# Performance work log

Measured on AMD Instinct MI355X. Metric: run time of the kernel, lower is better.

Reference implementation:

```python
import jax, jax.numpy as jnp
import numpy as np

BZ, T, D, DFF, E, BEAMS = 128, 32, 768, 3072, 8, 2


def setup_inputs() -> dict:
    key = jax.random.key(0)
    ks = jax.random.split(key, 4)
    s = 0.02
    return {
        "x": jax.random.normal(ks[0], (BZ, T, D), jnp.float32),
        "attention_mask": jnp.ones((BZ, T), jnp.float32),
        "Wg": jax.random.normal(ks[1], (D, E), jnp.float32) * s,   # gate Linear(D,E,bias=False)
        "W1": jax.random.normal(ks[2], (E, D, DFF), jnp.float32) * s,
        "b1": jnp.zeros((E, DFF), jnp.float32),
        "W2": jax.random.normal(ks[3], (E, DFF, D), jnp.float32) * s,
        "b2": jnp.zeros((E, D), jnp.float32),
    }


def reference(x, attention_mask, Wg, W1, b1, W2, b2):
    # forward_gate: module builds its own all-ones mask regardless of input mask
    mask = jnp.ones((x.shape[0], x.shape[1]), x.dtype)
    x_avg = (x * mask[..., None]).sum(1) / mask[..., None].sum(1)   # [bz, D]
    prob = jax.nn.softmax(x_avg @ Wg, axis=-1)                       # [bz, E]
    # beam_search (layer_judge='first', pre-route): topk on exp(log(softmax)) == softmax probs
    scores = jnp.exp(jnp.log(prob))
    topv, topi = jax.lax.top_k(scores, BEAMS)                        # [bz, beams]
    beam_scores = topv.reshape(-1)                                   # [bz*beams]
    expert_route = topi.reshape(-1, 1)                                # [bz*beams, 1]
    sel = expert_route[:, -1]
    # replicate x per beam: [bz*beams, T, D]
    x_rep = jnp.broadcast_to(x[:, None], (x.shape[0], BEAMS, x.shape[1], x.shape[2]))
    x_rep = x_rep.reshape(-1, x.shape[1], x.shape[2])
    # per-sample expert FFN dispatch (dense masked loop over the E=8 experts)
    out = jnp.zeros_like(x_rep)
    for e in range(E):
        h = jax.nn.gelu(jnp.einsum('nsd,df->nsf', x_rep, W1[e]) + b1[e], approximate=False)
        ye = jnp.einsum('nsf,fd->nsd', h, W2[e]) + b2[e]
        out = jnp.where((sel == e)[:, None, None], ye, out)
    return (out, beam_scores, expert_route)
```

## Files before the change

### kernel.cpp

```cpp
#include <hip/hip_runtime.h>
#include <cstddef>
#include <cstdint>

#define BZd   128
#define Td    32
#define Dd    768
#define DFFd  3072
#define Ed    8
#define NBEAM 256
#define ROWS_TOT 8192
#define OUT_ELEMS 6291456
#define MAXTILES 72
#define MAXT2    40

typedef unsigned short u16;
typedef __attribute__((ext_vector_type(4))) unsigned short ushort4v;
typedef __attribute__((ext_vector_type(8))) short frag_ab;
typedef __attribute__((ext_vector_type(4))) float floatx4;

__device__ __forceinline__ u16 f2bf(float f) {
  unsigned int u = __builtin_bit_cast(unsigned int, f);
  u += 0x7FFFu + ((u >> 16) & 1u);
  return (u16)(u >> 16);
}

__device__ __forceinline__ void async_copy16(u16* lds, const u16* g) {
  __builtin_amdgcn_global_load_lds(
      (const __attribute__((address_space(1))) void*)g,
      (__attribute__((address_space(3))) void*)lds, 16, 0, 0);
}

__device__ __forceinline__ float gelu_fast(float x) {
  float z = 1.5957691216f * (x + 0.044715f * x * x * x);
  return x / (1.0f + __expf(-z));
}

__global__ __launch_bounds__(256) void route_kernel(
    const float* __restrict__ x, const float* __restrict__ Wg,
    float* __restrict__ out, int* __restrict__ sel) {
  int b = blockIdx.x;
  int t = threadIdx.x;
  __shared__ float red[256][8];
  float la[8];
#pragma unroll
  for (int e = 0; e < 8; e++) la[e] = 0.f;
  for (int d = t; d < Dd; d += 256) {
    const float* xp = x + (size_t)b * Td * Dd + d;
    float xa = 0.f;
#pragma unroll
    for (int tt = 0; tt < Td; tt++) xa += xp[(size_t)tt * Dd];
    xa *= (1.0f / 32.0f);
#pragma unroll
    for (int e = 0; e < 8; e++) la[e] += xa * Wg[d * 8 + e];
  }
#pragma unroll
  for (int e = 0; e < 8; e++) red[t][e] = la[e];
  __syncthreads();
  for (int s = 128; s > 0; s >>= 1) {
    if (t < s) {
#pragma unroll
      for (int e = 0; e < 8; e++) red[t][e] += red[t + s][e];
    }
    __syncthreads();
  }
  if (t == 0) {
    float lg[8];
#pragma unroll
    for (int e = 0; e < 8; e++) lg[e] = red[0][e];
    float mx = lg[0];
#pragma unroll
    for (int e = 1; e < 8; e++) mx = fmaxf(mx, lg[e]);
    float p[8];
    float sum = 0.f;
#pragma unroll
    for (int e = 0; e < 8; e++) { p[e] = __expf(lg[e] - mx); sum += p[e]; }
    float inv = 1.0f / sum;
#pragma unroll
    for (int e = 0; e < 8; e++) p[e] *= inv;
    int i0 = 0; float v0 = p[0];
#pragma unroll
    for (int e = 1; e < 8; e++) if (p[e] > v0) { v0 = p[e]; i0 = e; }
    int i1 = -1; float v1 = -1.0f;
#pragma unroll
    for (int e = 0; e < 8; e++) if (e != i0 && p[e] > v1) { v1 = p[e]; i1 = e; }
    float* bs = out + OUT_ELEMS;
    float* er = out + OUT_ELEMS + NBEAM;
    bs[2 * b] = v0; bs[2 * b + 1] = v1;
    er[2 * b] = (float)i0; er[2 * b + 1] = (float)i1;
    sel[2 * b] = i0; sel[2 * b + 1] = i1;
  }
}

__global__ __launch_bounds__(256) void bucket_kernel(
    const int* __restrict__ sel, int* __restrict__ perm,
    int4* __restrict__ tiles, int4* __restrict__ tiles2) {
  __shared__ int ssel[NBEAM];
  __shared__ int scnt[8];
  __shared__ int soff[8];
  __shared__ int scur[8];
  __shared__ int sperm[NBEAM];
  int t = threadIdx.x;
  ssel[t] = sel[t];
  __syncthreads();
  if (t == 0) {
    for (int e = 0; e < 8; e++) scnt[e] = 0;
    for (int n = 0; n < NBEAM; n++) scnt[ssel[n]]++;
    int o = 0;
    for (int e = 0; e < 8; e++) { soff[e] = o; scur[e] = o; o += scnt[e]; }
    for (int n = 0; n < NBEAM; n++) { int e = ssel[n]; sperm[scur[e]++] = n; }
    int tt = 0;
    for (int e = 0; e < 8; e++) {
      int nr = scnt[e] * 32;
      int base = soff[e] * 32;
      for (int r0 = 0; r0 < nr; r0 += 128) {
        tiles[tt] = make_int4(e, base + r0, min(128, nr - r0), 0);
        tt++;
      }
    }
    for (; tt < MAXTILES; tt++) tiles[tt] = make_int4(-1, 0, 0, 0);
    int t2 = 0;
    for (int e = 0; e < 8; e++) {
      int nr = scnt[e] * 32;
      int base = soff[e] * 32;
      for (int r0 = 0; r0 < nr; r0 += 256) {
        tiles2[t2] = make_int4(e, base + r0, min(256, nr - r0), 0);
        t2++;
      }
    }
    for (; t2 < MAXT2; t2++) tiles2[t2] = make_int4(-1, 0, 0, 0);
  }
  __syncthreads();
  perm[t] = sperm[t];
}

__global__ __launch_bounds__(256) void convert_x_kernel(
    const float* __restrict__ x, u16* __restrict__ xbf) {
  size_t i = ((size_t)blockIdx.x * 256 + threadIdx.x) * 4;
  float4 v = *(const float4*)(x + i);
  ushort4v pv = {f2bf(v.x), f2bf(v.y), f2bf(v.z), f2bf(v.w)};
  *(ushort4v*)(xbf + i) = pv;
}

__global__ __launch_bounds__(256) void transpose_bf16_kernel(
    const float* __restrict__ in, u16* __restrict__ out, int row0, int col0,
    int ld_in, size_t estr_in, int ld_out, size_t estr_out) {
  __shared__ u16 tile[64][65];
  int e = blockIdx.z;
  int r0 = blockIdx.x * 64, c0 = blockIdx.y * 64;
  int t = threadIdx.x;
  int rr = t >> 4, cc4 = (t & 15) * 4;
  const float* ip = in + (size_t)e * estr_in + (size_t)(row0 + r0) * ld_in + col0 + c0;
#pragma unroll
  for (int i = 0; i < 4; i++) {
    int r = rr + 16 * i;
    float4 v = *(const float4*)(ip + (size_t)r * ld_in + cc4);
    tile[r][cc4 + 0] = f2bf(v.x);
    tile[r][cc4 + 1] = f2bf(v.y);
    tile[r][cc4 + 2] = f2bf(v.z);
    tile[r][cc4 + 3] = f2bf(v.w);
  }
  __syncthreads();
  int ccw = t >> 4, r4 = (t & 15) * 4;
  u16* op = out + (size_t)e * estr_out + (size_t)c0 * ld_out + r0;
#pragma unroll
  for (int i = 0; i < 4; i++) {
    int cc = ccw + 16 * i;
    ushort4v pv = {tile[r4 + 0][cc], tile[r4 + 1][cc], tile[r4 + 2][cc], tile[r4 + 3][cc]};
    *(ushort4v*)(op + (size_t)cc * ld_out + r4) = pv;
  }
}

__global__ __launch_bounds__(512, 2) void gemm1_kernel(
    const u16* __restrict__ xbf, const u16* __restrict__ w1t,
    const float* __restrict__ b1, const int* __restrict__ perm,
    const int4* __restrict__ tiles2, u16* __restrict__ h, int f0, int FC) {
  int4 meta = tiles2[blockIdx.y];
  int e = meta.x;
  if (e < 0) return;
  int grow0 = meta.y, nrows = meta.z;
  int bx = blockIdx.x;

  extern __shared__ __align__(16) u16 smem[];
  u16* As = smem;
  u16* Bs = smem + 32768;

  int t = threadIdx.x;
  int l = t & 63;
  int wid = t >> 6;
  int wr = wid >> 2;
  int wc = wid & 3;
  int lrow = l & 15, lquad = l >> 4;

  const u16* ag[4]; const u16* bg[4];
  int ldst[4];
#pragma unroll
  for (int j = 0; j < 4; j++) {
    int s = j * 512 + t;
    int m = s >> 3;
    int koff = ((s & 7) ^ ((m >> 1) & 7)) * 8;
    int gr = grow0 + m;
    int bidx = gr >> 5; bidx = bidx < NBEAM ? bidx : NBEAM - 1;
    int batch = perm[bidx] >> 1;
    ag[j] = xbf + ((size_t)batch * Td + (m & 31)) * Dd + koff;
    bg[j] = w1t + ((size_t)e * FC + bx * 256 + m) * Dd + koff;
    ldst[j] = j * 4096 + t * 8;
  }

  int swz = (lrow >> 1) & 7;
  int ca0 = (lquad ^ swz) * 8, ca1 = ((lquad + 4) ^ swz) * 8;
  int abase0 = (wr * 128 + lrow) * 64 + ca0;
  int abase1 = (wr * 128 + lrow) * 64 + ca1;
  int bbase0 = (wc * 64 + lrow) * 64 + ca0;
  int bbase1 = (wc * 64 + lrow) * 64 + ca1;

  floatx4 acc[8][4];
#pragma unroll
  for (int mi = 0; mi < 8; mi++)
#pragma unroll
    for (int ni = 0; ni < 4; ni++) acc[mi][ni] = (floatx4){0.f, 0.f, 0.f, 0.f};

  const int nk = Dd / 64;

#pragma unroll
  for (int j = 0; j < 4; j++) { async_copy16(As + ldst[j], ag[j]); ag[j] += 64; }
#pragma unroll
  for (int j = 0; j < 4; j++) { async_copy16(Bs + ldst[j], bg[j]); bg[j] += 64; }

  for (int kt = 0; kt < nk; kt++) {
    const int b = kt & 1;
    const u16* Ab = As + b * 16384;
    const u16* Bb = Bs + b * 16384;
    const int pd = (b ^ 1) * 16384;
    const bool pre = (kt + 1 < nk);

    frag_ab af[4], bfr[4];

    if (pre) {
      async_copy16(As + pd + ldst[0], ag[0]); ag[0] += 64;
      async_copy16(As + pd + ldst[1], ag[1]); ag[1] += 64;
      asm volatile("s_waitcnt vmcnt(2)\n\ts_barrier" ::: "memory");
    } else {
      asm volatile("s_waitcnt vmcnt(0)\n\ts_barrier" ::: "memory");
    }
#pragma unroll
    for (int i = 0; i < 4; i++) bfr[i] = *(const frag_ab*)(Bb + bbase0 + i * 1024);
#pragma unroll
    for (int i = 0; i < 4; i++) af[i] = *(const frag_ab*)(Ab + abase0 + i * 1024);
    __builtin_amdgcn_s_setprio(1);
#pragma unroll
    for (int mi = 0; mi < 4; mi++)
#pragma unroll
      for (int ni = 0; ni < 4; ni++)
        acc[mi][ni] = __builtin_amdgcn_mfma_f32_16x16x32_bf16(bfr[ni], af[mi], acc[mi][ni], 0, 0, 0);
    __builtin_amdgcn_s_setprio(0);

    if (pre) {
      async_copy16(As + pd + ldst[2], ag[2]); ag[2] += 64;
      async_copy16(As + pd + ldst[3], ag[3]); ag[3] += 64;
    }
#pragma unroll
    for (int i = 0; i < 4; i++) af[i] = *(const frag_ab*)(Ab + abase0 + (i + 4) * 1024);
    __builtin_amdgcn_s_setprio(1);
#pragma unroll
    for (int mi = 0; mi < 4; mi++)
#pragma unroll
      for (int ni = 0; ni < 4; ni++)
        acc[mi + 4][ni] = __builtin_amdgcn_mfma_f32_16x16x32_bf16(bfr[ni], af[mi], acc[mi + 4][ni], 0, 0, 0);
    __builtin_amdgcn_s_setprio(0);

    if (pre) {
      async_copy16(Bs + pd + ldst[0], bg[0]); bg[0] += 64;
      async_copy16(Bs + pd + ldst[1], bg[1]); bg[1] += 64;
    }
#pragma unroll
    for (int i = 0; i < 4; i++) bfr[i] = *(const frag_ab*)(Bb + bbase1 + i * 1024);
#pragma unroll
    for (int i = 0; i < 4; i++) af[i] = *(const frag_ab*)(Ab + abase1 + i * 1024);
    __builtin_amdgcn_s_setprio(1);
#pragma unroll
    for (int mi = 0; mi < 4; mi++)
#pragma unroll
      for (int ni = 0; ni < 4; ni++)
        acc[mi][ni] = __builtin_amdgcn_mfma_f32_16x16x32_bf16(bfr[ni], af[mi], acc[mi][ni], 0, 0, 0);
    __builtin_amdgcn_s_setprio(0);

    if (pre) {
      async_copy16(Bs + pd + ldst[2], bg[2]); bg[2] += 64;
      async_copy16(Bs + pd + ldst[3], bg[3]); bg[3] += 64;
    }
#pragma unroll
    for (int i = 0; i < 4; i++) af[i] = *(const frag_ab*)(Ab + abase1 + (i + 4) * 1024);
    __builtin_amdgcn_s_setprio(1);
#pragma unroll
    for (int mi = 0; mi < 4; mi++)
#pragma unroll
      for (int ni = 0; ni < 4; ni++)
        acc[mi + 4][ni] = __builtin_amdgcn_mfma_f32_16x16x32_bf16(bfr[ni], af[mi], acc[mi + 4][ni], 0, 0, 0);
    __builtin_amdgcn_s_setprio(0);

    asm volatile("s_barrier" ::: "memory");
  }

#pragma unroll
  for (int mi = 0; mi < 8; mi++) {
    int row = wr * 128 + mi * 16 + lrow;
    if (row < nrows) {
      u16* hp = h + (size_t)(grow0 + row) * FC + bx * 256 + wc * 64 + lquad * 4;
      const float* bp = b1 + (size_t)e * DFFd + f0 + bx * 256 + wc * 64 + lquad * 4;
#pragma unroll
      for (int ni = 0; ni < 4; ni++) {
        float4 bias = *(const float4*)(bp + ni * 16);
        ushort4v pv = {f2bf(gelu_fast(acc[mi][ni][0] + bias.x)),
                       f2bf(gelu_fast(acc[mi][ni][1] + bias.y)),
                       f2bf(gelu_fast(acc[mi][ni][2] + bias.z)),
                       f2bf(gelu_fast(acc[mi][ni][3] + bias.w))};
        *(ushort4v*)(hp + ni * 16) = pv;
      }
    }
  }
}

__global__ __launch_bounds__(512, 2) void gemm2_kernel(
    const u16* __restrict__ h, const u16* __restrict__ w2t,
    const float* __restrict__ b2, const int* __restrict__ perm,
    const int4* __restrict__ tiles2, float* __restrict__ out,
    float* __restrict__ part, int FC, int first) {
  int4 meta = tiles2[blockIdx.y];
  int e = meta.x;
  if (e < 0) return;
  int grow0 = meta.y, nrows = meta.z;
  int bx = blockIdx.x;
  int kz = blockIdx.z;
  const int KC = FC / (int)gridDim.z;

  extern __shared__ __align__(16) u16 smem[];
  u16* As = smem;
  u16* Bs = smem + 32768;
  __shared__ int sbeam[8];

  int t = threadIdx.x;
  if (t < 8) {
    int idx = (grow0 >> 5) + t;
    sbeam[t] = perm[idx < NBEAM ? idx : NBEAM - 1];
  }
  __syncthreads();

  int l = t & 63;
  int wid = t >> 6;
  int wr = wid >> 2;
  int wc = wid & 3;
  int lrow = l & 15, lquad = l >> 4;

  const u16* ag[4]; const u16* bg[4];
  int ldst[4];
#pragma unroll
  for (int j = 0; j < 4; j++) {
    int s = j * 512 + t;
    int m = s >> 3;
    int koff = ((s & 7) ^ ((m >> 1) & 7)) * 8;
    int arow = grow0 + m;
    arow = arow < ROWS_TOT ? arow : ROWS_TOT - 1;
    ag[j] = h + (size_t)arow * FC + kz * KC + koff;
    bg[j] = w2t + ((size_t)e * Dd + bx * 256 + m) * FC + kz * KC + koff;
    ldst[j] = j * 4096 + t * 8;
  }

  int swz = (lrow >> 1) & 7;
  int ca0 = (lquad ^ swz) * 8, ca1 = ((lquad + 4) ^ swz) * 8;
  int abase0 = (wr * 128 + lrow) * 64 + ca0;
  int abase1 = (wr * 128 + lrow) * 64 + ca1;
  int bbase0 = (wc * 64 + lrow) * 64 + ca0;
  int bbase1 = (wc * 64 + lrow) * 64 + ca1;

  floatx4 acc[8][4];
#pragma unroll
  for (int mi = 0; mi < 8; mi++)
#pragma unroll
    for (int ni = 0; ni < 4; ni++) acc[mi][ni] = (floatx4){0.f, 0.f, 0.f, 0.f};

  const int nk = KC / 64;

#pragma unroll
  for (int j = 0; j < 4; j++) { async_copy16(As + ldst[j], ag[j]); ag[j] += 64; }
#pragma unroll
  for (int j = 0; j < 4; j++) { async_copy16(Bs + ldst[j], bg[j]); bg[j] += 64; }

  for (int kt = 0; kt < nk; kt++) {
    const int b = kt & 1;
    const u16* Ab = As + b * 16384;
    const u16* Bb = Bs + b * 16384;
    const int pd = (b ^ 1) * 16384;
    const bool pre = (kt + 1 < nk);

    frag_ab af[4], bfr[4];

    if (pre) {
      async_copy16(As + pd + ldst[0], ag[0]); ag[0] += 64;
      async_copy16(As + pd + ldst[1], ag[1]); ag[1] += 64;
      asm volatile("s_waitcnt vmcnt(2)\n\ts_barrier" ::: "memory");
    } else {
      asm volatile("s_waitcnt vmcnt(0)\n\ts_barrier" ::: "memory");
    }
#pragma unroll
    for (int i = 0; i < 4; i++) bfr[i] = *(const frag_ab*)(Bb + bbase0 + i * 1024);
#pragma unroll
    for (int i = 0; i < 4; i++) af[i] = *(const frag_ab*)(Ab + abase0 + i * 1024);
    __builtin_amdgcn_s_setprio(1);
#pragma unroll
    for (int mi = 0; mi < 4; mi++)
#pragma unroll
      for (int ni = 0; ni < 4; ni++)
        acc[mi][ni] = __builtin_amdgcn_mfma_f32_16x16x32_bf16(bfr[ni], af[mi], acc[mi][ni], 0, 0, 0);
    __builtin_amdgcn_s_setprio(0);

    if (pre) {
      async_copy16(As + pd + ldst[2], ag[2]); ag[2] += 64;
      async_copy16(As + pd + ldst[3], ag[3]); ag[3] += 64;
    }
#pragma unroll
    for (int i = 0; i < 4; i++) af[i] = *(const frag_ab*)(Ab + abase0 + (i + 4) * 1024);
    __builtin_amdgcn_s_setprio(1);
#pragma unroll
    for (int mi = 0; mi < 4; mi++)
#pragma unroll
      for (int ni = 0; ni < 4; ni++)
        acc[mi + 4][ni] = __builtin_amdgcn_mfma_f32_16x16x32_bf16(bfr[ni], af[mi], acc[mi + 4][ni], 0, 0, 0);
    __builtin_amdgcn_s_setprio(0);

    if (pre) {
      async_copy16(Bs + pd + ldst[0], bg[0]); bg[0] += 64;
      async_copy16(Bs + pd + ldst[1], bg[1]); bg[1] += 64;
    }
#pragma unroll
    for (int i = 0; i < 4; i++) bfr[i] = *(const frag_ab*)(Bb + bbase1 + i * 1024);
#pragma unroll
    for (int i = 0; i < 4; i++) af[i] = *(const frag_ab*)(Ab + abase1 + i * 1024);
    __builtin_amdgcn_s_setprio(1);
#pragma unroll
    for (int mi = 0; mi < 4; mi++)
#pragma unroll
      for (int ni = 0; ni < 4; ni++)
        acc[mi][ni] = __builtin_amdgcn_mfma_f32_16x16x32_bf16(bfr[ni], af[mi], acc[mi][ni], 0, 0, 0);
    __builtin_amdgcn_s_setprio(0);

    if (pre) {
      async_copy16(Bs + pd + ldst[2], bg[2]); bg[2] += 64;
      async_copy16(Bs + pd + ldst[3], bg[3]); bg[3] += 64;
    }
#pragma unroll
    for (int i = 0; i < 4; i++) af[i] = *(const frag_ab*)(Ab + abase1 + (i + 4) * 1024);
    __builtin_amdgcn_s_setprio(1);
#pragma unroll
    for (int mi = 0; mi < 4; mi++)
#pragma unroll
      for (int ni = 0; ni < 4; ni++)
        acc[mi + 4][ni] = __builtin_amdgcn_mfma_f32_16x16x32_bf16(bfr[ni], af[mi], acc[mi + 4][ni], 0, 0, 0);
    __builtin_amdgcn_s_setprio(0);

    asm volatile("s_barrier" ::: "memory");
  }

#pragma unroll
  for (int mi = 0; mi < 8; mi++) {
    int row = wr * 128 + mi * 16 + lrow;
    if (row < nrows) {
      int beam = sbeam[row >> 5];
      size_t base = ((size_t)beam * Td + (row & 31)) * Dd + bx * 256 + wc * 64 + lquad * 4;
      float* op = (kz == 0 ? out : part) + base;
      const float* bp = b2 + (size_t)e * Dd + bx * 256 + wc * 64 + lquad * 4;
#pragma unroll
      for (int ni = 0; ni < 4; ni++) {
        if (first) {
          float4 v = {acc[mi][ni][0], acc[mi][ni][1], acc[mi][ni][2], acc[mi][ni][3]};
          if (kz == 0) {
            float4 bias = *(const float4*)(bp + ni * 16);
            v.x += bias.x; v.y += bias.y; v.z += bias.z; v.w += bias.w;
          }
          *(float4*)(op + ni * 16) = v;
        } else {
          float4 o = *(float4*)(op + ni * 16);
          o.x += acc[mi][ni][0]; o.y += acc[mi][ni][1];
          o.z += acc[mi][ni][2]; o.w += acc[mi][ni][3];
          *(float4*)(op + ni * 16) = o;
        }
      }
    }
  }
}

__global__ __launch_bounds__(256) void reduce_kernel(
    float* __restrict__ out, const float* __restrict__ part) {
  size_t i = ((size_t)blockIdx.x * 256 + threadIdx.x) * 4;
  float4 o = *(float4*)(out + i);
  float4 p = *(const float4*)(part + i);
  o.x += p.x; o.y += p.y; o.z += p.z; o.w += p.w;
  *(float4*)(out + i) = o;
}

extern "C" void kernel_launch(void* const* d_in, const int* in_sizes, int n_in,
                              void* d_out, int out_size, void* d_ws, size_t ws_size,
                              hipStream_t stream) {
  const float* x  = (const float*)d_in[0];
  const float* Wg = (const float*)d_in[2];
  const float* W1 = (const float*)d_in[3];
  const float* b1 = (const float*)d_in[4];
  const float* W2 = (const float*)d_in[5];
  const float* b2 = (const float*)d_in[6];
  float* out = (float*)d_out;

  char* ws = (char*)d_ws;
  int*  sel    = (int*)ws;
  int*  perm   = sel + NBEAM;
  int4* tiles  = (int4*)(ws + 4096);
  int4* tiles2 = (int4*)(ws + 6144);

  const size_t xbf_off = 65536;
  const size_t xbf_bytes = (size_t)BZd * Td * Dd * 2;
  int FC = 768;
  if      (xbf_off + xbf_bytes + (size_t)40960 * 3072 <= ws_size) FC = 3072;
  else if (xbf_off + xbf_bytes + (size_t)40960 * 1536 <= ws_size) FC = 1536;
  int NC = DFFd / FC;

  u16* xbf = (u16*)(ws + xbf_off);
  u16* w1t = (u16*)(ws + xbf_off + xbf_bytes);
  u16* w2t = w1t + (size_t)Ed * FC * Dd;
  u16* h   = w2t + (size_t)Ed * Dd * FC;

  const size_t part_off = xbf_off + xbf_bytes + (size_t)40960 * FC;
  const size_t part_bytes = (size_t)OUT_ELEMS * 4;
  int SPLIT = (part_off + part_bytes <= ws_size) ? 2 : 1;
  float* part = (float*)(ws + part_off);

  static bool attr_done = false;
  if (!attr_done) {
    hipFuncSetAttribute(reinterpret_cast<const void*>(gemm1_kernel),
                        hipFuncAttributeMaxDynamicSharedMemorySize, 131072);
    hipFuncSetAttribute(reinterpret_cast<const void*>(gemm2_kernel),
                        hipFuncAttributeMaxDynamicSharedMemorySize, 131072);
    attr_done = true;
  }

  route_kernel<<<BZd, 256, 0, stream>>>(x, Wg, out, sel);
  bucket_kernel<<<1, 256, 0, stream>>>(sel, perm, tiles, tiles2);
  convert_x_kernel<<<(BZd * Td * Dd) / 1024, 256, 0, stream>>>(x, xbf);

  for (int c = 0; c < NC; c++) {
    transpose_bf16_kernel<<<dim3(Dd / 64, FC / 64, Ed), 256, 0, stream>>>(
        W1, w1t, 0, c * FC, DFFd, (size_t)Dd * DFFd, Dd, (size_t)FC * Dd);
    transpose_bf16_kernel<<<dim3(FC / 64, Dd / 64, Ed), 256, 0, stream>>>(
        W2, w2t, c * FC, 0, Dd, (size_t)DFFd * Dd, FC, (size_t)Dd * FC);
    gemm1_kernel<<<dim3(FC / 256, MAXT2), 512, 131072, stream>>>(
        xbf, w1t, b1, perm, tiles2, h, c * FC, FC);
    gemm2_kernel<<<dim3(Dd / 256, MAXT2, SPLIT), 512, 131072, stream>>>(
        h, w2t, b2, perm, tiles2, out, part, FC, c == 0 ? 1 : 0);
  }
  if (SPLIT == 2)
    reduce_kernel<<<OUT_ELEMS / 1024, 256, 0, stream>>>(out, part);
}
```

Baseline: 371.7 us.

## Use 1024-thread GEMM blocks, merge weight transposes, fuse x conversion into routing

The two expert GEMM kernels now run 16 waves per block instead of 8. Each wave owns a 64x64 output sub-tile rather than 128x64, which halves the accumulator registers per thread and doubles the number of waves available to hide latency for the same 256x256 tile. The W1 and W2 transposes are merged into one launch, and the fp32-to-bf16 conversion of x moves into the routing kernel, removing two kernel launches. The risks are higher LDS barrier contention and a longer tail in the routing kernel, which now also streams the full activation tensor.

Result: faster. 364.1 us (-2.1%).

```diff
diff --git a/kernel.cpp b/kernel.cpp
--- a/kernel.cpp
+++ b/kernel.cpp
@@ -37,7 +37,7 @@
 
 __global__ __launch_bounds__(256) void route_kernel(
     const float* __restrict__ x, const float* __restrict__ Wg,
-    float* __restrict__ out, int* __restrict__ sel) {
+    float* __restrict__ out, int* __restrict__ sel, u16* __restrict__ xbf) {
   int b = blockIdx.x;
   int t = threadIdx.x;
   __shared__ float red[256][8];
@@ -89,11 +89,18 @@
     er[2 * b] = (float)i0; er[2 * b + 1] = (float)i1;
     sel[2 * b] = i0; sel[2 * b + 1] = i1;
   }
+  const float* xs = x + (size_t)b * Td * Dd;
+  u16* xd = xbf + (size_t)b * Td * Dd;
+  for (int i = t; i < Td * Dd / 4; i += 256) {
+    float4 v = *(const float4*)(xs + (size_t)i * 4);
+    ushort4v pv = {f2bf(v.x), f2bf(v.y), f2bf(v.z), f2bf(v.w)};
+    *(ushort4v*)(xd + (size_t)i * 4) = pv;
+  }
 }
 
 __global__ __launch_bounds__(256) void bucket_kernel(
     const int* __restrict__ sel, int* __restrict__ perm,
-    int4* __restrict__ tiles, int4* __restrict__ tiles2) {
+    int4* __restrict__ tiles2) {
   __shared__ int ssel[NBEAM];
   __shared__ int scnt[8];
   __shared__ int soff[8];
@@ -108,16 +115,6 @@
     int o = 0;
     for (int e = 0; e < 8; e++) { soff[e] = o; scur[e] = o; o += scnt[e]; }
     for (int n = 0; n < NBEAM; n++) { int e = ssel[n]; sperm[scur[e]++] = n; }
-    int tt = 0;
-    for (int e = 0; e < 8; e++) {
-      int nr = scnt[e] * 32;
-      int base = soff[e] * 32;
-      for (int r0 = 0; r0 < nr; r0 += 128) {
-        tiles[tt] = make_int4(e, base + r0, min(128, nr - r0), 0);
-        tt++;
-      }
-    }
-    for (; tt < MAXTILES; tt++) tiles[tt] = make_int4(-1, 0, 0, 0);
     int t2 = 0;
     for (int e = 0; e < 8; e++) {
       int nr = scnt[e] * 32;
@@ -133,20 +130,27 @@
   perm[t] = sperm[t];
 }
 
-__global__ __launch_bounds__(256) void convert_x_kernel(
-    const float* __restrict__ x, u16* __restrict__ xbf) {
-  size_t i = ((size_t)blockIdx.x * 256 + threadIdx.x) * 4;
-  float4 v = *(const float4*)(x + i);
-  ushort4v pv = {f2bf(v.x), f2bf(v.y), f2bf(v.z), f2bf(v.w)};
-  *(ushort4v*)(xbf + i) = pv;
-}
-
-__global__ __launch_bounds__(256) void transpose_bf16_kernel(
-    const float* __restrict__ in, u16* __restrict__ out, int row0, int col0,
-    int ld_in, size_t estr_in, int ld_out, size_t estr_out) {
+__global__ __launch_bounds__(256) void transpose2_kernel(
+    const float* __restrict__ W1, const float* __restrict__ W2,
+    u16* __restrict__ w1t, u16* __restrict__ w2t, int c, int FC) {
   __shared__ u16 tile[64][65];
-  int e = blockIdx.z;
-  int r0 = blockIdx.x * 64, c0 = blockIdx.y * 64;
+  int z = blockIdx.z;
+  const float* in; u16* out;
+  int e, r0, c0, row0, col0, ld_in, ld_out;
+  size_t estr_in, estr_out;
+  if (z < 8) {
+    e = z; in = W1; out = w1t;
+    row0 = 0; col0 = c * FC; ld_in = DFFd; estr_in = (size_t)Dd * DFFd;
+    ld_out = Dd; estr_out = (size_t)FC * Dd;
+    r0 = blockIdx.y * 64;
+    c0 = blockIdx.x * 64;
+  } else {
+    e = z - 8; in = W2; out = w2t;
+    row0 = c * FC; col0 = 0; ld_in = Dd; estr_in = (size_t)DFFd * Dd;
+    ld_out = FC; estr_out = (size_t)Dd * FC;
+    r0 = blockIdx.x * 64;
+    c0 = blockIdx.y * 64;
+  }
   int t = threadIdx.x;
   int rr = t >> 4, cc4 = (t & 15) * 4;
   const float* ip = in + (size_t)e * estr_in + (size_t)(row0 + r0) * ld_in + col0 + c0;
@@ -170,7 +174,7 @@
   }
 }
 
-__global__ __launch_bounds__(512, 2) void gemm1_kernel(
+__global__ __launch_bounds__(1024, 4) void gemm1_kernel(
     const u16* __restrict__ xbf, const u16* __restrict__ w1t,
     const float* __restrict__ b1, const int* __restrict__ perm,
     const int4* __restrict__ tiles2, u16* __restrict__ h, int f0, int FC) {
@@ -191,40 +195,39 @@
   int wc = wid & 3;
   int lrow = l & 15, lquad = l >> 4;
 
-  const u16* ag[4]; const u16* bg[4];
-  int ldst[4];
-#pragma unroll
-  for (int j = 0; j < 4; j++) {
-    int s = j * 512 + t;
+  const u16* ag[2]; const u16* bg[2];
+  int ldst[2];
+#pragma unroll
+  for (int j = 0; j < 2; j++) {
+    int s = j * 1024 + t;
     int m = s >> 3;
     int koff = ((s & 7) ^ ((m >> 1) & 7)) * 8;
-    int gr = grow0 + m;
-    int bidx = gr >> 5; bidx = bidx < NBEAM ? bidx : NBEAM - 1;
+    int bidx = (grow0 + m) >> 5; bidx = bidx < NBEAM ? bidx : NBEAM - 1;
     int batch = perm[bidx] >> 1;
     ag[j] = xbf + ((size_t)batch * Td + (m & 31)) * Dd + koff;
     bg[j] = w1t + ((size_t)e * FC + bx * 256 + m) * Dd + koff;
-    ldst[j] = j * 4096 + t * 8;
+    ldst[j] = s * 8;
   }
 
   int swz = (lrow >> 1) & 7;
   int ca0 = (lquad ^ swz) * 8, ca1 = ((lquad + 4) ^ swz) * 8;
-  int abase0 = (wr * 128 + lrow) * 64 + ca0;
-  int abase1 = (wr * 128 + lrow) * 64 + ca1;
+  int abase0 = (wr * 64 + lrow) * 64 + ca0;
+  int abase1 = (wr * 64 + lrow) * 64 + ca1;
   int bbase0 = (wc * 64 + lrow) * 64 + ca0;
   int bbase1 = (wc * 64 + lrow) * 64 + ca1;
 
-  floatx4 acc[8][4];
-#pragma unroll
-  for (int mi = 0; mi < 8; mi++)
+  floatx4 acc[4][4];
+#pragma unroll
+  for (int mi = 0; mi < 4; mi++)
 #pragma unroll
     for (int ni = 0; ni < 4; ni++) acc[mi][ni] = (floatx4){0.f, 0.f, 0.f, 0.f};
 
   const int nk = Dd / 64;
 
-#pragma unroll
-  for (int j = 0; j < 4; j++) { async_copy16(As + ldst[j], ag[j]); ag[j] += 64; }
-#pragma unroll
-  for (int j = 0; j < 4; j++) { async_copy16(Bs + ldst[j], bg[j]); bg[j] += 64; }
+  async_copy16(As + ldst[0], ag[0]); ag[0] += 64;
+  async_copy16(Bs + ldst[0], bg[0]); bg[0] += 64;
+  async_copy16(As + ldst[1], ag[1]); ag[1] += 64;
+  async_copy16(Bs + ldst[1], bg[1]); bg[1] += 64;
 
   for (int kt = 0; kt < nk; kt++) {
     const int b = kt & 1;
@@ -233,11 +236,11 @@
     const int pd = (b ^ 1) * 16384;
     const bool pre = (kt + 1 < nk);
 
-    frag_ab af[4], bfr[4];
+    frag_ab af[2], bfr[4];
 
     if (pre) {
       async_copy16(As + pd + ldst[0], ag[0]); ag[0] += 64;
-      async_copy16(As + pd + ldst[1], ag[1]); ag[1] += 64;
+      async_copy16(Bs + pd + ldst[0], bg[0]); bg[0] += 64;
       asm volatile("s_waitcnt vmcnt(2)\n\ts_barrier" ::: "memory");
     } else {
       asm volatile("s_waitcnt vmcnt(0)\n\ts_barrier" ::: "memory");
@@ -245,65 +248,57 @@
 #pragma unroll
     for (int i = 0; i < 4; i++) bfr[i] = *(const frag_ab*)(Bb + bbase0 + i * 1024);
 #pragma unroll
-    for (int i = 0; i < 4; i++) af[i] = *(const frag_ab*)(Ab + abase0 + i * 1024);
-    __builtin_amdgcn_s_setprio(1);
-#pragma unroll
-    for (int mi = 0; mi < 4; mi++)
+    for (int i = 0; i < 2; i++) af[i] = *(const frag_ab*)(Ab + abase0 + i * 1024);
+    __builtin_amdgcn_s_setprio(1);
+#pragma unroll
+    for (int mi = 0; mi < 2; mi++)
 #pragma unroll
       for (int ni = 0; ni < 4; ni++)
         acc[mi][ni] = __builtin_amdgcn_mfma_f32_16x16x32_bf16(bfr[ni], af[mi], acc[mi][ni], 0, 0, 0);
     __builtin_amdgcn_s_setprio(0);
 
     if (pre) {
-      async_copy16(As + pd + ldst[2], ag[2]); ag[2] += 64;
-      async_copy16(As + pd + ldst[3], ag[3]); ag[3] += 64;
-    }
-#pragma unroll
-    for (int i = 0; i < 4; i++) af[i] = *(const frag_ab*)(Ab + abase0 + (i + 4) * 1024);
-    __builtin_amdgcn_s_setprio(1);
-#pragma unroll
-    for (int mi = 0; mi < 4; mi++)
-#pragma unroll
-      for (int ni = 0; ni < 4; ni++)
-        acc[mi + 4][ni] = __builtin_amdgcn_mfma_f32_16x16x32_bf16(bfr[ni], af[mi], acc[mi + 4][ni], 0, 0, 0);
-    __builtin_amdgcn_s_setprio(0);
-
-    if (pre) {
-      async_copy16(Bs + pd + ldst[0], bg[0]); bg[0] += 64;
+      async_copy16(As + pd + ldst[1], ag[1]); ag[1] += 64;
       async_copy16(Bs + pd + ldst[1], bg[1]); bg[1] += 64;
     }
 #pragma unroll
+    for (int i = 0; i < 2; i++) af[i] = *(const frag_ab*)(Ab + abase0 + (i + 2) * 1024);
+    __builtin_amdgcn_s_setprio(1);
+#pragma unroll
+    for (int mi = 0; mi < 2; mi++)
+#pragma unroll
+      for (int ni = 0; ni < 4; ni++)
+        acc[mi + 2][ni] = __builtin_amdgcn_mfma_f32_16x16x32_bf16(bfr[ni], af[mi], acc[mi + 2][ni], 0, 0, 0);
+    __builtin_amdgcn_s_setprio(0);
+
+#pragma unroll
     for (int i = 0; i < 4; i++) bfr[i] = *(const frag_ab*)(Bb + bbase1 + i * 1024);
 #pragma unroll
-    for (int i = 0; i < 4; i++) af[i] = *(const frag_ab*)(Ab + abase1 + i * 1024);
-    __builtin_amdgcn_s_setprio(1);
-#pragma unroll
-    for (int mi = 0; mi < 4; mi++)
+    for (int i = 0; i < 2; i++) af[i] = *(const frag_ab*)(Ab + abase1 + i * 1024);
+    __builtin_amdgcn_s_setprio(1);
+#pragma unroll
+    for (int mi = 0; mi < 2; mi++)
 #pragma unroll
       for (int ni = 0; ni < 4; ni++)
         acc[mi][ni] = __builtin_amdgcn_mfma_f32_16x16x32_bf16(bfr[ni], af[mi], acc[mi][ni], 0, 0, 0);
     __builtin_amdgcn_s_setprio(0);
 
-    if (pre) {
-      async_copy16(Bs + pd + ldst[2], bg[2]); bg[2] += 64;
-      async_copy16(Bs + pd + ldst[3], bg[3]); bg[3] += 64;
-    }
-#pragma unroll
-    for (int i = 0; i < 4; i++) af[i] = *(const frag_ab*)(Ab + abase1 + (i + 4) * 1024);
-    __builtin_amdgcn_s_setprio(1);
-#pragma unroll
-    for (int mi = 0; mi < 4; mi++)
-#pragma unroll
-      for (int ni = 0; ni < 4; ni++)
-        acc[mi + 4][ni] = __builtin_amdgcn_mfma_f32_16x16x32_bf16(bfr[ni], af[mi], acc[mi + 4][ni], 0, 0, 0);
+#pragma unroll
+    for (int i = 0; i < 2; i++) af[i] = *(const frag_ab*)(Ab + abase1 + (i + 2) * 1024);
+    __builtin_amdgcn_s_setprio(1);
+#pragma unroll
+    for (int mi = 0; mi < 2; mi++)
+#pragma unroll
+      for (int ni = 0; ni < 4; ni++)
+        acc[mi + 2][ni] = __builtin_amdgcn_mfma_f32_16x16x32_bf16(bfr[ni], af[mi], acc[mi + 2][ni], 0, 0, 0);
     __builtin_amdgcn_s_setprio(0);
 
     asm volatile("s_barrier" ::: "memory");
   }
 
 #pragma unroll
-  for (int mi = 0; mi < 8; mi++) {
-    int row = wr * 128 + mi * 16 + lrow;
+  for (int mi = 0; mi < 4; mi++) {
+    int row = wr * 64 + mi * 16 + lrow;
     if (row < nrows) {
       u16* hp = h + (size_t)(grow0 + row) * FC + bx * 256 + wc * 64 + lquad * 4;
       const float* bp = b1 + (size_t)e * DFFd + f0 + bx * 256 + wc * 64 + lquad * 4;
@@ -320,7 +315,7 @@
   }
 }
 
-__global__ __launch_bounds__(512, 2) void gemm2_kernel(
+__global__ __launch_bounds__(1024, 4) void gemm2_kernel(
     const u16* __restrict__ h, const u16* __restrict__ w2t,
     const float* __restrict__ b2, const int* __restrict__ perm,
     const int4* __restrict__ tiles2, float* __restrict__ out,
@@ -351,39 +346,39 @@
   int wc = wid & 3;
   int lrow = l & 15, lquad = l >> 4;
 
-  const u16* ag[4]; const u16* bg[4];
-  int ldst[4];
-#pragma unroll
-  for (int j = 0; j < 4; j++) {
-    int s = j * 512 + t;
+  const u16* ag[2]; const u16* bg[2];
+  int ldst[2];
+#pragma unroll
+  for (int j = 0; j < 2; j++) {
+    int s = j * 1024 + t;
     int m = s >> 3;
     int koff = ((s & 7) ^ ((m >> 1) & 7)) * 8;
     int arow = grow0 + m;
     arow = arow < ROWS_TOT ? arow : ROWS_TOT - 1;
     ag[j] = h + (size_t)arow * FC + kz * KC + koff;
     bg[j] = w2t + ((size_t)e * Dd + bx * 256 + m) * FC + kz * KC + koff;
-    ldst[j] = j * 4096 + t * 8;
+    ldst[j] = s * 8;
   }
 
   int swz = (lrow >> 1) & 7;
   int ca0 = (lquad ^ swz) * 8, ca1 = ((lquad + 4) ^ swz) * 8;
-  int abase0 = (wr * 128 + lrow) * 64 + ca0;
-  int abase1 = (wr * 128 + lrow) * 64 + ca1;
+  int abase0 = (wr * 64 + lrow) * 64 + ca0;
+  int abase1 = (wr * 64 + lrow) * 64 + ca1;
   int bbase0 = (wc * 64 + lrow) * 64 + ca0;
   int bbase1 = (wc * 64 + lrow) * 64 + ca1;
 
-  floatx4 acc[8][4];
-#pragma unroll
-  for (int mi = 0; mi < 8; mi++)
+  floatx4 acc[4][4];
+#pragma unroll
+  for (int mi = 0; mi < 4; mi++)
 #pragma unroll
     for (int ni = 0; ni < 4; ni++) acc[mi][ni] = (floatx4){0.f, 0.f, 0.f, 0.f};
 
   const int nk = KC / 64;
 
-#pragma unroll
-  for (int j = 0; j < 4; j++) { async_copy16(As + ldst[j], ag[j]); ag[j] += 64; }
-#pragma unroll
-  for (int j = 0; j < 4; j++) { async_copy16(Bs + ldst[j], bg[j]); bg[j] += 64; }
+  async_copy16(As + ldst[0], ag[0]); ag[0] += 64;
+  async_copy16(Bs + ldst[0], bg[0]); bg[0] += 64;
+  async_copy16(As + ldst[1], ag[1]); ag[1] += 64;
+  async_copy16(Bs + ldst[1], bg[1]); bg[1] += 64;
 
   for (int kt = 0; kt < nk; kt++) {
     const int b = kt & 1;
@@ -392,11 +387,11 @@
     const int pd = (b ^ 1) * 16384;
     const bool pre = (kt + 1 < nk);
 
-    frag_ab af[4], bfr[4];
+    frag_ab af[2], bfr[4];
 
     if (pre) {
       async_copy16(As + pd + ldst[0], ag[0]); ag[0] += 64;
-      async_copy16(As + pd + ldst[1], ag[1]); ag[1] += 64;
+      async_copy16(Bs + pd + ldst[0], bg[0]); bg[0] += 64;
       asm volatile("s_waitcnt vmcnt(2)\n\ts_barrier" ::: "memory");
     } else {
       asm volatile("s_waitcnt vmcnt(0)\n\ts_barrier" ::: "memory");
@@ -404,65 +399,57 @@
 #pragma unroll
     for (int i = 0; i < 4; i++) bfr[i] = *(const frag_ab*)(Bb + bbase0 + i * 1024);
 #pragma unroll
-    for (int i = 0; i < 4; i++) af[i] = *(const frag_ab*)(Ab + abase0 + i * 1024);
-    __builtin_amdgcn_s_setprio(1);
-#pragma unroll
-    for (int mi = 0; mi < 4; mi++)
+    for (int i = 0; i < 2; i++) af[i] = *(const frag_ab*)(Ab + abase0 + i * 1024);
+    __builtin_amdgcn_s_setprio(1);
+#pragma unroll
+    for (int mi = 0; mi < 2; mi++)
 #pragma unroll
       for (int ni = 0; ni < 4; ni++)
         acc[mi][ni] = __builtin_amdgcn_mfma_f32_16x16x32_bf16(bfr[ni], af[mi], acc[mi][ni], 0, 0, 0);
     __builtin_amdgcn_s_setprio(0);
 
     if (pre) {
-      async_copy16(As + pd + ldst[2], ag[2]); ag[2] += 64;
-      async_copy16(As + pd + ldst[3], ag[3]); ag[3] += 64;
-    }
-#pragma unroll
-    for (int i = 0; i < 4; i++) af[i] = *(const frag_ab*)(Ab + abase0 + (i + 4) * 1024);
-    __builtin_amdgcn_s_setprio(1);
-#pragma unroll
-    for (int mi = 0; mi < 4; mi++)
-#pragma unroll
-      for (int ni = 0; ni < 4; ni++)
-        acc[mi + 4][ni] = __builtin_amdgcn_mfma_f32_16x16x32_bf16(bfr[ni], af[mi], acc[mi + 4][ni], 0, 0, 0);
-    __builtin_amdgcn_s_setprio(0);
-
-    if (pre) {
-      async_copy16(Bs + pd + ldst[0], bg[0]); bg[0] += 64;
+      async_copy16(As + pd + ldst[1], ag[1]); ag[1] += 64;
       async_copy16(Bs + pd + ldst[1], bg[1]); bg[1] += 64;
     }
 #pragma unroll
+    for (int i = 0; i < 2; i++) af[i] = *(const frag_ab*)(Ab + abase0 + (i + 2) * 1024);
+    __builtin_amdgcn_s_setprio(1);
+#pragma unroll
+    for (int mi = 0; mi < 2; mi++)
+#pragma unroll
+      for (int ni = 0; ni < 4; ni++)
+        acc[mi + 2][ni] = __builtin_amdgcn_mfma_f32_16x16x32_bf16(bfr[ni], af[mi], acc[mi + 2][ni], 0, 0, 0);
+    __builtin_amdgcn_s_setprio(0);
+
+#pragma unroll
     for (int i = 0; i < 4; i++) bfr[i] = *(const frag_ab*)(Bb + bbase1 + i * 1024);
 #pragma unroll
-    for (int i = 0; i < 4; i++) af[i] = *(const frag_ab*)(Ab + abase1 + i * 1024);
-    __builtin_amdgcn_s_setprio(1);
-#pragma unroll
-    for (int mi = 0; mi < 4; mi++)
+    for (int i = 0; i < 2; i++) af[i] = *(const frag_ab*)(Ab + abase1 + i * 1024);
+    __builtin_amdgcn_s_setprio(1);
+#pragma unroll
+    for (int mi = 0; mi < 2; mi++)
 #pragma unroll
       for (int ni = 0; ni < 4; ni++)
         acc[mi][ni] = __builtin_amdgcn_mfma_f32_16x16x32_bf16(bfr[ni], af[mi], acc[mi][ni], 0, 0, 0);
     __builtin_amdgcn_s_setprio(0);
 
-    if (pre) {
-      async_copy16(Bs + pd + ldst[2], bg[2]); bg[2] += 64;
-      async_copy16(Bs + pd + ldst[3], bg[3]); bg[3] += 64;
-    }
-#pragma unroll
-    for (int i = 0; i < 4; i++) af[i] = *(const frag_ab*)(Ab + abase1 + (i + 4) * 1024);
-    __builtin_amdgcn_s_setprio(1);
-#pragma unroll
-    for (int mi = 0; mi < 4; mi++)
-#pragma unroll
-      for (int ni = 0; ni < 4; ni++)
-        acc[mi + 4][ni] = __builtin_amdgcn_mfma_f32_16x16x32_bf16(bfr[ni], af[mi], acc[mi + 4][ni], 0, 0, 0);
+#pragma unroll
+    for (int i = 0; i < 2; i++) af[i] = *(const frag_ab*)(Ab + abase1 + (i + 2) * 1024);
+    __builtin_amdgcn_s_setprio(1);
+#pragma unroll
+    for (int mi = 0; mi < 2; mi++)
+#pragma unroll
+      for (int ni = 0; ni < 4; ni++)
+        acc[mi + 2][ni] = __builtin_amdgcn_mfma_f32_16x16x32_bf16(bfr[ni], af[mi], acc[mi + 2][ni], 0, 0, 0);
     __builtin_amdgcn_s_setprio(0);
 
     asm volatile("s_barrier" ::: "memory");
   }
 
 #pragma unroll
-  for (int mi = 0; mi < 8; mi++) {
-    int row = wr * 128 + mi * 16 + lrow;
+  for (int mi = 0; mi < 4; mi++) {
+    int row = wr * 64 + mi * 16 + lrow;
     if (row < nrows) {
       int beam = sbeam[row >> 5];
       size_t base = ((size_t)beam * Td + (row & 31)) * Dd + bx * 256 + wc * 64 + lquad * 4;
@@ -511,7 +498,6 @@
   char* ws = (char*)d_ws;
   int*  sel    = (int*)ws;
   int*  perm   = sel + NBEAM;
-  int4* tiles  = (int4*)(ws + 4096);
   int4* tiles2 = (int4*)(ws + 6144);
 
   const size_t xbf_off = 65536;
@@ -540,18 +526,15 @@
     attr_done = true;
   }
 
-  route_kernel<<<BZd, 256, 0, stream>>>(x, Wg, out, sel);
-  bucket_kernel<<<1, 256, 0, stream>>>(sel, perm, tiles, tiles2);
-  convert_x_kernel<<<(BZd * Td * Dd) / 1024, 256, 0, stream>>>(x, xbf);
+  route_kernel<<<BZd, 256, 0, stream>>>(x, Wg, out, sel, xbf);
+  bucket_kernel<<<1, 256, 0, stream>>>(sel, perm, tiles2);
 
   for (int c = 0; c < NC; c++) {
-    transpose_bf16_kernel<<<dim3(Dd / 64, FC / 64, Ed), 256, 0, stream>>>(
-        W1, w1t, 0, c * FC, DFFd, (size_t)Dd * DFFd, Dd, (size_t)FC * Dd);
-    transpose_bf16_kernel<<<dim3(FC / 64, Dd / 64, Ed), 256, 0, stream>>>(
-        W2, w2t, c * FC, 0, Dd, (size_t)DFFd * Dd, FC, (size_t)Dd * FC);
-    gemm1_kernel<<<dim3(FC / 256, MAXT2), 512, 131072, stream>>>(
+    transpose2_kernel<<<dim3(FC / 64, Dd / 64, 2 * Ed), 256, 0, stream>>>(
+        W1, W2, w1t, w2t, c, FC);
+    gemm1_kernel<<<dim3(FC / 256, MAXT2), 1024, 131072, stream>>>(
         xbf, w1t, b1, perm, tiles2, h, c * FC, FC);
-    gemm2_kernel<<<dim3(Dd / 256, MAXT2, SPLIT), 512, 131072, stream>>>(
+    gemm2_kernel<<<dim3(Dd / 256, MAXT2, SPLIT), 1024, 131072, stream>>>(
         h, w2t, b2, perm, tiles2, out, part, FC, c == 0 ? 1 : 0);
   }
   if (SPLIT == 2)
```
